# Optimization experiments

Measured on AMD Instinct MI355X. Metric: run time of the kernel, lower is better.

## Reference

```python
import jax, jax.numpy as jnp
import numpy as np

BLOCK_SIZE = 256
NEG = -10000.0  # matches the module's additive mask constant (not -inf)

def setup_inputs() -> dict:
    key = jax.random.key(0)
    qkv = jax.random.normal(key, (4, 4096, 192), dtype=jnp.float32)
    return {"qkv": qkv}

def reference(qkv):
    B, S, dm = qkv.shape
    d = dm // 3
    q, k, v = qkv[..., :d], qkv[..., d:2*d], qkv[..., 2*d:]
    scale = 1.0 / jnp.sqrt(jnp.asarray(d, dtype=qkv.dtype))
    scores = jnp.einsum('bqd,bkd->bqk', q, k * scale)  # [B,S,S]
    i = jnp.arange(S)[:, None]
    j = jnp.arange(S)[None, :]
    # allowed: i - block_size <= j <= i ; else additive -10000 (as in torch code)
    mask = jnp.where((j <= i) & (j >= i - BLOCK_SIZE), 0.0, NEG).astype(scores.dtype)
    attn = jax.nn.softmax(scores + mask[None, :, :], axis=-1)
    return jnp.einsum('bqk,bkd->bqd', attn, v)
```

## Files before the change

kernel.cpp:

```cpp
#include <hip/hip_runtime.h>
#include <hip/hip_bf16.h>


#define LOG2E 1.4426950408889634f

typedef __attribute__((ext_vector_type(8))) short  frag;
typedef __attribute__((ext_vector_type(4))) float  f32x4;

static __device__ inline short f2bf(float x) {
    __hip_bfloat16 h = __float2bfloat16(x);
    return __builtin_bit_cast(short, h);
}

#define DPPF(x, ctrl) __builtin_bit_cast(float, \
    __builtin_amdgcn_mov_dpp(__builtin_bit_cast(int, (x)), (ctrl), 0xF, 0xF, true))

static __device__ inline float red16_max(float x) {
    x = fmaxf(x, DPPF(x, 0xB1));
    x = fmaxf(x, DPPF(x, 0x4E));
    x = fmaxf(x, DPPF(x, 0x141));
    x = fmaxf(x, DPPF(x, 0x140));
    return x;
}
static __device__ inline float red16_sum(float x) {
    x += DPPF(x, 0xB1);
    x += DPPF(x, 0x4E);
    x += DPPF(x, 0x141);
    x += DPPF(x, 0x140);
    return x;
}

#define LSTR 70
#define PSTR 42
#define OSTR 65

__global__ __launch_bounds__(512, 2) void swa_mfma8(const float* __restrict__ qkv,
                                                    float* __restrict__ out)
{
    __shared__ short Qs[64 * LSTR];
    __shared__ short Ks[64 * LSTR];
    __shared__ short Vt[64 * LSTR];
    __shared__ short Pw[8][16 * PSTR];
    __shared__ float Om[4][16 * OSTR];
    __shared__ float2 mlbuf[4][16];

    const int b    = blockIdx.y;
    const int q0   = blockIdx.x * 64;
    const int t    = threadIdx.x;
    const int w    = t >> 6;
    const int s    = w & 3;
    const int g    = w >> 2;
    const int lane = t & 63;
    const int cl   = lane & 15;
    const int quad = lane >> 4;
    const int ql   = 4 * quad;

    const float4* qkv4 = (const float4*)qkv;
    const int r_st = t >> 3;
    const int c8   = t & 7;

    {
        const size_t base = (size_t)(b * 4096 + q0 + r_st) * 48;
        #pragma unroll
        for (int i = 0; i < 2; ++i) {
            float4 v = qkv4[base + c8 + 8 * i];
            short4 s4 = { f2bf(v.x * 0.125f), f2bf(v.y * 0.125f),
                          f2bf(v.z * 0.125f), f2bf(v.w * 0.125f) };
            *(short4*)&Qs[r_st * LSTR + 4 * (c8 + 8 * i)] = s4;
        }
    }

    const int c0 = (q0 >= 256) ? 0 : (4 - (q0 >> 6));

    float4 preK[2], preV[2];
    {
        const int kb = q0 - 256 + 64 * c0;
        const size_t base = (size_t)(b * 4096 + kb + r_st) * 48;
        #pragma unroll
        for (int i = 0; i < 2; ++i) {
            preK[i] = qkv4[base + 16 + c8 + 8 * i];
            preV[i] = qkv4[base + 32 + c8 + 8 * i];
        }
    }

    __syncthreads();
    const frag qf0 = *(const frag*)&Qs[(16 * s + cl) * LSTR + 8 * quad];
    const frag qf1 = *(const frag*)&Qs[(16 * s + cl) * LSTR + 32 + 8 * quad];

    float m[4], l[4];
    f32x4 oacc[4];
    #pragma unroll
    for (int r = 0; r < 4; ++r) { m[r] = -1e30f; l[r] = 0.f; }
    #pragma unroll
    for (int n4 = 0; n4 < 4; ++n4) oacc[n4] = (f32x4){0.f, 0.f, 0.f, 0.f};

    for (int c = c0; c < 5; ++c) {
        __syncthreads();

        #pragma unroll
        for (int i = 0; i < 2; ++i) {
            short4 k4 = { f2bf(preK[i].x), f2bf(preK[i].y),
                          f2bf(preK[i].z), f2bf(preK[i].w) };
            *(short4*)&Ks[r_st * LSTR + 4 * (c8 + 8 * i)] = k4;
            const int d0 = 4 * (c8 + 8 * i);
            Vt[(d0 + 0) * LSTR + r_st] = f2bf(preV[i].x);
            Vt[(d0 + 1) * LSTR + r_st] = f2bf(preV[i].y);
            Vt[(d0 + 2) * LSTR + r_st] = f2bf(preV[i].z);
            Vt[(d0 + 3) * LSTR + r_st] = f2bf(preV[i].w);
        }
        __syncthreads();

        if (c < 4) {
            const int kb = q0 - 256 + 64 * (c + 1);
            const size_t base = (size_t)(b * 4096 + kb + r_st) * 48;
            #pragma unroll
            for (int i = 0; i < 2; ++i) {
                preK[i] = qkv4[base + 16 + c8 + 8 * i];
                preV[i] = qkv4[base + 32 + c8 + 8 * i];
            }
        }

        f32x4 sc[2];
        #pragma unroll
        for (int u = 0; u < 2; ++u) {
            const int t4 = 2 * g + u;
            sc[u] = (f32x4){0.f, 0.f, 0.f, 0.f};
            const frag kf0 = *(const frag*)&Ks[(16 * t4 + cl) * LSTR + 8 * quad];
            const frag kf1 = *(const frag*)&Ks[(16 * t4 + cl) * LSTR + 32 + 8 * quad];
            sc[u] = __builtin_amdgcn_mfma_f32_16x16x32_bf16(qf0, kf0, sc[u], 0, 0, 0);
            sc[u] = __builtin_amdgcn_mfma_f32_16x16x32_bf16(qf1, kf1, sc[u], 0, 0, 0);
        }

        if (c == 4) {
            #pragma unroll
            for (int u = 0; u < 2; ++u) {
                const int t4 = 2 * g + u;
                #pragma unroll
                for (int r = 0; r < 4; ++r)
                    if (16 * s + ql + r < 16 * t4 + cl) sc[u][r] = -1e30f;
            }
        } else if (c == 0) {
            #pragma unroll
            for (int u = 0; u < 2; ++u) {
                const int t4 = 2 * g + u;
                #pragma unroll
                for (int r = 0; r < 4; ++r)
                    if (16 * s + ql + r > 16 * t4 + cl) sc[u][r] = -1e30f;
            }
        }

        #pragma unroll
        for (int r = 0; r < 4; ++r) {
            float mx = red16_max(fmaxf(sc[0][r], sc[1][r]));
            const float mnew  = fmaxf(m[r], mx);
            const float alpha = __builtin_amdgcn_exp2f((m[r] - mnew) * LOG2E);
            m[r] = mnew;
            float sum = 0.f;
            #pragma unroll
            for (int u = 0; u < 2; ++u) {
                float p = (sc[u][r] <= -1e29f)
                            ? 0.f
                            : __builtin_amdgcn_exp2f((sc[u][r] - mnew) * LOG2E);
                Pw[w][(ql + r) * PSTR + 16 * u + cl] = f2bf(p);
                sum += p;
            }
            l[r] = l[r] * alpha + red16_sum(sum);
            #pragma unroll
            for (int n4 = 0; n4 < 4; ++n4) oacc[n4][r] *= alpha;
        }

        const frag pf = *(const frag*)&Pw[w][cl * PSTR + 8 * quad];
        #pragma unroll
        for (int n4 = 0; n4 < 4; ++n4) {
            const frag vf = *(const frag*)&Vt[(16 * n4 + cl) * LSTR + 32 * g + 8 * quad];
            oacc[n4] = __builtin_amdgcn_mfma_f32_16x16x32_bf16(pf, vf, oacc[n4], 0, 0, 0);
        }
    }

    if (g == 1) {
        #pragma unroll
        for (int n4 = 0; n4 < 4; ++n4)
            #pragma unroll
            for (int r = 0; r < 4; ++r)
                Om[s][(ql + r) * OSTR + 16 * n4 + cl] = oacc[n4][r];
        if (cl == 0)
            #pragma unroll
            for (int r = 0; r < 4; ++r)
                mlbuf[s][ql + r] = make_float2(m[r], l[r]);
    }
    __syncthreads();
    if (g == 0) {
        #pragma unroll
        for (int r = 0; r < 4; ++r) {
            const float2 ml1 = mlbuf[s][ql + r];
            const float M  = fmaxf(m[r], ml1.x);
            const float a0 = __builtin_amdgcn_exp2f((m[r]  - M) * LOG2E);
            const float a1 = __builtin_amdgcn_exp2f((ml1.x - M) * LOG2E);
            const float L  = l[r] * a0 + ml1.y * a1;
            const float inv = 1.0f / L;
            const size_t row = (size_t)(b * 4096 + q0 + 16 * s + ql + r) * 64;
            #pragma unroll
            for (int n4 = 0; n4 < 4; ++n4) {
                const float o1 = Om[s][(ql + r) * OSTR + 16 * n4 + cl];
                out[row + 16 * n4 + cl] = (oacc[n4][r] * a0 + o1 * a1) * inv;
            }
        }
    }
}

extern "C" void kernel_launch(void* const* d_in, const int* in_sizes, int n_in,
                              void* d_out, int out_size, void* d_ws, size_t ws_size,
                              hipStream_t stream) {
    const float* qkv = (const float*)d_in[0];
    float* out = (float*)d_out;
    dim3 grid(64, 4);
    dim3 block(512);
    hipLaunchKernelGGL(swa_mfma8, grid, block, 0, stream, qkv, out);
}
```

Baseline: 67.82 us.

## Compute transposed scores so softmax is per-lane and P stays in registers

Swaps the MFMA operands so each lane holds one query row's scores, which turns the row max and sum into in-lane reductions plus two cross-lane shuffles instead of DPP reductions over four rows. The probability tile is packed to bf16 and rearranged with shuffles into the B-operand layout, removing the shared-memory round trip through Pw. The epilogue now writes float4 outputs and uses a repacked Om layout. The cost is extra shuffle and select work and a more complex data layout.

After: 67.41 us. About the same (-0.6%).

```diff
diff --git a/kernel.cpp b/kernel.cpp
--- a/kernel.cpp
+++ b/kernel.cpp
@@ -11,37 +11,21 @@
     __hip_bfloat16 h = __float2bfloat16(x);
     return __builtin_bit_cast(short, h);
 }
-
-#define DPPF(x, ctrl) __builtin_bit_cast(float, \
-    __builtin_amdgcn_mov_dpp(__builtin_bit_cast(int, (x)), (ctrl), 0xF, 0xF, true))
-
-static __device__ inline float red16_max(float x) {
-    x = fmaxf(x, DPPF(x, 0xB1));
-    x = fmaxf(x, DPPF(x, 0x4E));
-    x = fmaxf(x, DPPF(x, 0x141));
-    x = fmaxf(x, DPPF(x, 0x140));
-    return x;
-}
-static __device__ inline float red16_sum(float x) {
-    x += DPPF(x, 0xB1);
-    x += DPPF(x, 0x4E);
-    x += DPPF(x, 0x141);
-    x += DPPF(x, 0x140);
-    return x;
+static __device__ inline unsigned pkbf(float x, float y) {
+    return (unsigned)(unsigned short)__builtin_bit_cast(short, __float2bfloat16(x))
+         | ((unsigned)(unsigned short)__builtin_bit_cast(short, __float2bfloat16(y)) << 16);
 }
 
 #define LSTR 70
-#define PSTR 42
-#define OSTR 65
-
-__global__ __launch_bounds__(512, 2) void swa_mfma8(const float* __restrict__ qkv,
-                                                    float* __restrict__ out)
+#define OMS  17
+
+__global__ __launch_bounds__(512, 2) void swa_mfma11(const float* __restrict__ qkv,
+                                                     float* __restrict__ out)
 {
     __shared__ short Qs[64 * LSTR];
     __shared__ short Ks[64 * LSTR];
     __shared__ short Vt[64 * LSTR];
-    __shared__ short Pw[8][16 * PSTR];
-    __shared__ float Om[4][16 * OSTR];
+    __shared__ float Om[4][64 * OMS];
     __shared__ float2 mlbuf[4][16];
 
     const int b    = blockIdx.y;
@@ -54,6 +38,8 @@
     const int cl   = lane & 15;
     const int quad = lane >> 4;
     const int ql   = 4 * quad;
+    const int hb   = quad >> 1;
+    const int lb   = quad & 1;
 
     const float4* qkv4 = (const float4*)qkv;
     const int r_st = t >> 3;
@@ -87,10 +73,8 @@
     const frag qf0 = *(const frag*)&Qs[(16 * s + cl) * LSTR + 8 * quad];
     const frag qf1 = *(const frag*)&Qs[(16 * s + cl) * LSTR + 32 + 8 * quad];
 
-    float m[4], l[4];
+    float m = -1e30f, l = 0.f;
     f32x4 oacc[4];
-    #pragma unroll
-    for (int r = 0; r < 4; ++r) { m[r] = -1e30f; l[r] = 0.f; }
     #pragma unroll
     for (int n4 = 0; n4 < 4; ++n4) oacc[n4] = (f32x4){0.f, 0.f, 0.f, 0.f};
 
@@ -127,8 +111,8 @@
             sc[u] = (f32x4){0.f, 0.f, 0.f, 0.f};
             const frag kf0 = *(const frag*)&Ks[(16 * t4 + cl) * LSTR + 8 * quad];
             const frag kf1 = *(const frag*)&Ks[(16 * t4 + cl) * LSTR + 32 + 8 * quad];
-            sc[u] = __builtin_amdgcn_mfma_f32_16x16x32_bf16(qf0, kf0, sc[u], 0, 0, 0);
-            sc[u] = __builtin_amdgcn_mfma_f32_16x16x32_bf16(qf1, kf1, sc[u], 0, 0, 0);
+            sc[u] = __builtin_amdgcn_mfma_f32_16x16x32_bf16(kf0, qf0, sc[u], 0, 0, 0);
+            sc[u] = __builtin_amdgcn_mfma_f32_16x16x32_bf16(kf1, qf1, sc[u], 0, 0, 0);
         }
 
         if (c == 4) {
@@ -137,7 +121,7 @@
                 const int t4 = 2 * g + u;
                 #pragma unroll
                 for (int r = 0; r < 4; ++r)
-                    if (16 * s + ql + r < 16 * t4 + cl) sc[u][r] = -1e30f;
+                    if (16 * t4 + ql + r > 16 * s + cl) sc[u][r] = -1e30f;
             }
         } else if (c == 0) {
             #pragma unroll
@@ -145,35 +129,62 @@
                 const int t4 = 2 * g + u;
                 #pragma unroll
                 for (int r = 0; r < 4; ++r)
-                    if (16 * s + ql + r > 16 * t4 + cl) sc[u][r] = -1e30f;
-            }
-        }
-
-        #pragma unroll
-        for (int r = 0; r < 4; ++r) {
-            float mx = red16_max(fmaxf(sc[0][r], sc[1][r]));
-            const float mnew  = fmaxf(m[r], mx);
-            const float alpha = __builtin_amdgcn_exp2f((m[r] - mnew) * LOG2E);
-            m[r] = mnew;
-            float sum = 0.f;
-            #pragma unroll
-            for (int u = 0; u < 2; ++u) {
-                float p = (sc[u][r] <= -1e29f)
-                            ? 0.f
-                            : __builtin_amdgcn_exp2f((sc[u][r] - mnew) * LOG2E);
-                Pw[w][(ql + r) * PSTR + 16 * u + cl] = f2bf(p);
-                sum += p;
-            }
-            l[r] = l[r] * alpha + red16_sum(sum);
-            #pragma unroll
-            for (int n4 = 0; n4 < 4; ++n4) oacc[n4][r] *= alpha;
-        }
-
-        const frag pf = *(const frag*)&Pw[w][cl * PSTR + 8 * quad];
+                    if (16 * t4 + ql + r < 16 * s + cl) sc[u][r] = -1e30f;
+            }
+        }
+
+        float mx = fmaxf(fmaxf(fmaxf(sc[0][0], sc[0][1]), fmaxf(sc[0][2], sc[0][3])),
+                         fmaxf(fmaxf(sc[1][0], sc[1][1]), fmaxf(sc[1][2], sc[1][3])));
+        mx = fmaxf(mx, __shfl_xor(mx, 16));
+        mx = fmaxf(mx, __shfl_xor(mx, 32));
+        const float mnew  = fmaxf(m, mx);
+        const float alpha = __builtin_amdgcn_exp2f((m - mnew) * LOG2E);
+        m = mnew;
+        float p[8];
+        float sum = 0.f;
+        #pragma unroll
+        for (int u = 0; u < 2; ++u)
+            #pragma unroll
+            for (int r = 0; r < 4; ++r) {
+                const float pv = (sc[u][r] <= -1e29f)
+                                   ? 0.f
+                                   : __builtin_amdgcn_exp2f((sc[u][r] - mnew) * LOG2E);
+                p[4 * u + r] = pv;
+                sum += pv;
+            }
+        sum += __shfl_xor(sum, 16);
+        sum += __shfl_xor(sum, 32);
+        l = l * alpha + sum;
+        #pragma unroll
+        for (int n4 = 0; n4 < 4; ++n4) oacc[n4] *= alpha;
+
+        const unsigned a0 = pkbf(p[0], p[1]);
+        const unsigned a1 = pkbf(p[2], p[3]);
+        const unsigned a2 = pkbf(p[4], p[5]);
+        const unsigned a3 = pkbf(p[6], p[7]);
+        const unsigned u0s = hb == 0 ? a2 : a0;
+        const unsigned u1s = hb == 0 ? a3 : a1;
+        const unsigned r0 = __shfl_xor((int)u0s, 32);
+        const unsigned r1 = __shfl_xor((int)u1s, 32);
+        const unsigned cc0 = hb == 0 ? a0 : r0;
+        const unsigned cc1 = hb == 0 ? a1 : r1;
+        const unsigned cc2 = hb == 0 ? r0 : a2;
+        const unsigned cc3 = hb == 0 ? r1 : a3;
+        const unsigned v0 = lb == 0 ? cc2 : cc0;
+        const unsigned v1 = lb == 0 ? cc3 : cc1;
+        const unsigned w0 = __shfl_xor((int)v0, 16);
+        const unsigned w1 = __shfl_xor((int)v1, 16);
+        unsigned F[4];
+        F[0] = lb == 0 ? cc0 : w0;
+        F[1] = lb == 0 ? cc1 : w1;
+        F[2] = lb == 0 ? w0 : cc2;
+        F[3] = lb == 0 ? w1 : cc3;
+        const frag pfr = __builtin_bit_cast(frag, *(uint4*)F);
+
         #pragma unroll
         for (int n4 = 0; n4 < 4; ++n4) {
             const frag vf = *(const frag*)&Vt[(16 * n4 + cl) * LSTR + 32 * g + 8 * quad];
-            oacc[n4] = __builtin_amdgcn_mfma_f32_16x16x32_bf16(pf, vf, oacc[n4], 0, 0, 0);
+            oacc[n4] = __builtin_amdgcn_mfma_f32_16x16x32_bf16(vf, pfr, oacc[n4], 0, 0, 0);
         }
     }
 
@@ -182,28 +193,26 @@
         for (int n4 = 0; n4 < 4; ++n4)
             #pragma unroll
             for (int r = 0; r < 4; ++r)
-                Om[s][(ql + r) * OSTR + 16 * n4 + cl] = oacc[n4][r];
-        if (cl == 0)
-            #pragma unroll
-            for (int r = 0; r < 4; ++r)
-                mlbuf[s][ql + r] = make_float2(m[r], l[r]);
+                Om[s][lane * OMS + 4 * n4 + r] = oacc[n4][r];
+        if (quad == 0) mlbuf[s][cl] = make_float2(m, l);
     }
     __syncthreads();
     if (g == 0) {
-        #pragma unroll
-        for (int r = 0; r < 4; ++r) {
-            const float2 ml1 = mlbuf[s][ql + r];
-            const float M  = fmaxf(m[r], ml1.x);
-            const float a0 = __builtin_amdgcn_exp2f((m[r]  - M) * LOG2E);
-            const float a1 = __builtin_amdgcn_exp2f((ml1.x - M) * LOG2E);
-            const float L  = l[r] * a0 + ml1.y * a1;
-            const float inv = 1.0f / L;
-            const size_t row = (size_t)(b * 4096 + q0 + 16 * s + ql + r) * 64;
-            #pragma unroll
-            for (int n4 = 0; n4 < 4; ++n4) {
-                const float o1 = Om[s][(ql + r) * OSTR + 16 * n4 + cl];
-                out[row + 16 * n4 + cl] = (oacc[n4][r] * a0 + o1 * a1) * inv;
-            }
+        const float2 ml1 = mlbuf[s][cl];
+        const float M  = fmaxf(m, ml1.x);
+        const float a0 = __builtin_amdgcn_exp2f((m     - M) * LOG2E);
+        const float a1 = __builtin_amdgcn_exp2f((ml1.x - M) * LOG2E);
+        const float L  = l * a0 + ml1.y * a1;
+        const float inv = 1.0f / L;
+        const size_t row = (size_t)(b * 4096 + q0 + 16 * s + cl) * 64;
+        #pragma unroll
+        for (int n4 = 0; n4 < 4; ++n4) {
+            float4 o;
+            o.x = (oacc[n4][0] * a0 + Om[s][lane * OMS + 4 * n4 + 0] * a1) * inv;
+            o.y = (oacc[n4][1] * a0 + Om[s][lane * OMS + 4 * n4 + 1] * a1) * inv;
+            o.z = (oacc[n4][2] * a0 + Om[s][lane * OMS + 4 * n4 + 2] * a1) * inv;
+            o.w = (oacc[n4][3] * a0 + Om[s][lane * OMS + 4 * n4 + 3] * a1) * inv;
+            *(float4*)&out[row + 16 * n4 + ql] = o;
         }
     }
 }
@@ -215,5 +224,5 @@
     float* out = (float*)d_out;
     dim3 grid(64, 4);
     dim3 block(512);
-    hipLaunchKernelGGL(swa_mfma8, grid, block, 0, stream, qkv, out);
-}
+    hipLaunchKernelGGL(swa_mfma11, grid, block, 0, stream, qkv, out);
+}
```
